# Kernel optimization log

Measured on AMD Instinct MI355X. Metric: run time of the kernel, lower is better.

The kernel has to match this reference:

```python
import jax, jax.numpy as jnp
import numpy as np

DIM = 1024
NUM_HEADS = 16
HEAD_DIM = DIM // NUM_HEADS
SCALE = HEAD_DIM ** -0.5


def setup_inputs() -> dict:
    key = jax.random.key(0)
    k1, k2, k3, k4 = jax.random.split(key, 4)
    x = jax.random.normal(k1, (4, 2048, DIM), dtype=jnp.float32)
    # torch nn.Linear(dim, 3*dim, bias=False): weight shape [3*dim, dim]
    w_qkv = jax.random.normal(k2, (3 * DIM, DIM), dtype=jnp.float32) * (DIM ** -0.5)
    # torch nn.Linear(dim, dim): weight [dim, dim], bias [dim]
    w_proj = jax.random.normal(k3, (DIM, DIM), dtype=jnp.float32) * (DIM ** -0.5)
    b_proj = jax.random.normal(k4, (DIM,), dtype=jnp.float32) * 0.01
    return {"x": x, "w_qkv": w_qkv, "w_proj": w_proj, "b_proj": b_proj}


def reference(x, w_qkv, w_proj, b_proj):
    B, N, C = x.shape
    # qkv: [B, N, 3*C] -> [3, B, H, N, Dh]
    qkv = (x @ w_qkv.T).reshape(B, N, 3, NUM_HEADS, HEAD_DIM)
    qkv = jnp.transpose(qkv, (2, 0, 3, 1, 4))
    q, k, v = qkv[0], qkv[1], qkv[2]
    # full score matrix, as in the original module
    attn = jnp.einsum("bhqd,bhkd->bhqk", q, k) * SCALE
    attn = jax.nn.softmax(attn, axis=-1)
    out = jnp.einsum("bhqk,bhkd->bhqd", attn, v)  # [B,H,N,Dh]
    out = jnp.transpose(out, (0, 2, 1, 3)).reshape(B, N, C)
    return out @ w_proj.T + b_proj
```

## Files before the change

kernel.cpp:

```cpp
#include <hip/hip_runtime.h>
#include <stdint.h>

#define DIM 1024
#define SEQ 2048
#define BATCH 4
#define ROWS (BATCH*SEQ)
#define QSCALE 0.1803368801111f

typedef __attribute__((ext_vector_type(8))) short bf16x8;
typedef __attribute__((ext_vector_type(4))) float f32x4;
typedef __attribute__((ext_vector_type(8))) _Float16 f16x8;
typedef __attribute__((ext_vector_type(2))) __fp16 fp16x2_raw;

#if __has_builtin(__builtin_amdgcn_exp2f)
#define EXP2F(x) __builtin_amdgcn_exp2f(x)
#else
#define EXP2F(x) __expf((x) * 0.69314718056f)
#endif

#define MFMA_BF16_K32(a,b,c) __builtin_amdgcn_mfma_f32_16x16x32_bf16(a,b,c,0,0,0)
#define MFMA_F16_K32(a,b,c)  __builtin_amdgcn_mfma_f32_16x16x32_f16(a,b,c,0,0,0)

__device__ __forceinline__ unsigned short f2bf(float f) {
  union { float f; unsigned int u; } v; v.f = f;
  unsigned int u = v.u;
  return (unsigned short)((u + 0x7FFFu + ((u >> 16) & 1u)) >> 16);
}

__device__ __forceinline__ unsigned short f2h(float f) {
  union { _Float16 h; unsigned short u; } v;
  v.h = (_Float16)f;
  return v.u;
}

__device__ __forceinline__ unsigned int pkrtz_bits(float lo, float hi) {
  union { fp16x2_raw h; unsigned int u; } v;
  v.h = __builtin_amdgcn_cvt_pkrtz(lo, hi);
  return v.u;
}

__device__ __forceinline__ void gload_lds16(const void* g, void* l) {
  __builtin_amdgcn_global_load_lds(
      (const __attribute__((address_space(1))) unsigned int*)g,
      (__attribute__((address_space(3))) unsigned int*)l,
      16, 0, 0);
}

__global__ void cast_all(const float* __restrict__ x,
                         const float* __restrict__ wq,
                         const float* __restrict__ wp,
                         unsigned short* __restrict__ xb,
                         unsigned short* __restrict__ wqb,
                         unsigned short* __restrict__ wpb) {
  const int i = (blockIdx.x * blockDim.x + threadIdx.x) * 4;
  const float* src;
  unsigned short* dst;
  int off;
  if (i < ROWS * DIM)                 { src = x;  dst = xb;  off = i; }
  else if (i < ROWS * DIM + 3 * DIM * DIM) { src = wq; dst = wqb; off = i - ROWS * DIM; }
  else                                { src = wp; dst = wpb; off = i - ROWS * DIM - 3 * DIM * DIM; }
  float4 f = *(const float4*)(src + off);
  ushort4 o;
  o.x = f2bf(f.x); o.y = f2bf(f.y); o.z = f2bf(f.z); o.w = f2bf(f.w);
  *(ushort4*)(dst + off) = o;
}

template<int SWAP>
__device__ __forceinline__ f32x4 mm(bf16x8 a, bf16x8 b, f32x4 c) {
  if constexpr (SWAP) return __builtin_amdgcn_mfma_f32_16x16x32_bf16(b, a, c, 0, 0, 0);
  else                return __builtin_amdgcn_mfma_f32_16x16x32_bf16(a, b, c, 0, 0, 0);
}

template<int SWAP, int NTX>
__global__ __launch_bounds__(512, 2) void gemm_qkv8(
    const unsigned short* __restrict__ A,
    const unsigned short* __restrict__ W,
    unsigned short* __restrict__ qb,
    unsigned short* __restrict__ kb,
    unsigned short* __restrict__ vtb) {
  constexpr int K = DIM;
  constexpr int NT = K / 64;
  constexpr int N0B = SWAP ? 0 : 2048;
  __shared__ unsigned short Al[2][256 * 64];
  __shared__ unsigned short Bl[2][256 * 64];

  const int tid  = threadIdx.x;
  const int wave = tid >> 6, lane = tid & 63;
  const int quad = lane >> 4, l16 = lane & 15;
  const int wm = wave >> 2, wn = wave & 3;

  constexpr int nwg = NTX * 32;
  int id = blockIdx.y * NTX + blockIdx.x;
  id = (id & 7) * (nwg >> 3) + (id >> 3);
  const int bx = id % NTX, by = id / NTX;
  const int m0 = by * 256, n0 = N0B + bx * 256;

  const int srow8 = lane >> 3;
  const int schk  = (lane & 7) ^ srow8;
  const unsigned short* Ast = A + (size_t)(m0 + wave * 8 + srow8) * K + (schk << 3);
  const unsigned short* Bst = W + (size_t)(n0 + wave * 8 + srow8) * K + (schk << 3);

  auto stg = [&](const unsigned short* g, int R0, int kt, unsigned short* l) {
    gload_lds16((const void*)(g + (size_t)R0 * K + kt),
                (void*)(l + (R0 + wave * 8) * 64));
  };
  auto ldf = [&](const unsigned short* base, int rb, int idx, int kk) -> bf16x8 {
    const int r = rb + idx * 16 + l16;
    return *(const bf16x8*)&base[r * 64 + (((kk * 4 + quad) ^ (l16 & 7)) << 3)];
  };

  f32x4 acc[8][4];
#pragma unroll
  for (int i = 0; i < 8; ++i)
#pragma unroll
    for (int j = 0; j < 4; ++j) acc[i][j] = (f32x4)0.f;

  stg(Ast, 0, 0, Al[0]);  stg(Ast, 128, 0, Al[0]);
  stg(Ast, 64, 0, Al[0]); stg(Ast, 192, 0, Al[0]);
  stg(Bst, 0, 0, Bl[0]);  stg(Bst, 64, 0, Bl[0]);
  stg(Bst, 128, 0, Bl[0]); stg(Bst, 192, 0, Bl[0]);
  stg(Ast, 0, 64, Al[1]);  stg(Ast, 128, 64, Al[1]);
  stg(Bst, 0, 64, Bl[1]);  stg(Bst, 64, 64, Bl[1]);
  stg(Ast, 64, 64, Al[1]); stg(Ast, 192, 64, Al[1]);
  asm volatile("s_waitcnt vmcnt(6)" ::: "memory");
  __builtin_amdgcn_s_barrier();

  bf16x8 af[4][2], bf[4][2];
  int buf = 0;
  for (int t = 0; t < NT; ++t, buf ^= 1) {
    const unsigned short* Ac = Al[buf];
    const unsigned short* Bc = Bl[buf];
    unsigned short* Asg = Al[buf];
    unsigned short* Bsg = Bl[buf];
    const int kt2 = (t + 2) * 64;

#pragma unroll
    for (int mi = 0; mi < 4; ++mi) {
      af[mi][0] = ldf(Ac, wm * 128, mi, 0);
      af[mi][1] = ldf(Ac, wm * 128, mi, 1);
    }
#pragma unroll
    for (int ni = 0; ni < 2; ++ni) {
      bf[ni][0] = ldf(Bc, wn * 64, ni, 0);
      bf[ni][1] = ldf(Bc, wn * 64, ni, 1);
    }
    if (t + 1 < NT) {
      stg(Bst, 128, (t + 1) * 64, Bl[buf ^ 1]);
      stg(Bst, 192, (t + 1) * 64, Bl[buf ^ 1]);
    }
    __builtin_amdgcn_s_barrier();
    asm volatile("s_waitcnt lgkmcnt(0)" ::: "memory");
    __builtin_amdgcn_s_setprio(1);
#pragma unroll
    for (int mi = 0; mi < 4; ++mi)
#pragma unroll
      for (int ni = 0; ni < 2; ++ni)
#pragma unroll
        for (int kk = 0; kk < 2; ++kk)
          acc[mi][ni] = mm<SWAP>(af[mi][kk], bf[ni][kk], acc[mi][ni]);
    __builtin_amdgcn_s_setprio(0);
    __builtin_amdgcn_s_barrier();

#pragma unroll
    for (int ni = 2; ni < 4; ++ni) {
      bf[ni][0] = ldf(Bc, wn * 64, ni, 0);
      bf[ni][1] = ldf(Bc, wn * 64, ni, 1);
    }
    if (t + 2 < NT) {
      stg(Ast, 0, kt2, Asg);
      stg(Ast, 128, kt2, Asg);
    }
    __builtin_amdgcn_s_barrier();
    asm volatile("s_waitcnt lgkmcnt(0)" ::: "memory");
    __builtin_amdgcn_s_setprio(1);
#pragma unroll
    for (int mi = 0; mi < 4; ++mi)
#pragma unroll
      for (int ni = 2; ni < 4; ++ni)
#pragma unroll
        for (int kk = 0; kk < 2; ++kk)
          acc[mi][ni] = mm<SWAP>(af[mi][kk], bf[ni][kk], acc[mi][ni]);
    __builtin_amdgcn_s_setprio(0);
    __builtin_amdgcn_s_barrier();

#pragma unroll
    for (int mi = 0; mi < 4; ++mi) {
      af[mi][0] = ldf(Ac, wm * 128, mi + 4, 0);
      af[mi][1] = ldf(Ac, wm * 128, mi + 4, 1);
    }
    if (t + 2 < NT) {
      stg(Bst, 0, kt2, Bsg);
      stg(Bst, 64, kt2, Bsg);
    }
    __builtin_amdgcn_s_barrier();
    asm volatile("s_waitcnt lgkmcnt(0)" ::: "memory");
    __builtin_amdgcn_s_setprio(1);
#pragma unroll
    for (int mi = 0; mi < 4; ++mi)
#pragma unroll
      for (int ni = 2; ni < 4; ++ni)
#pragma unroll
        for (int kk = 0; kk < 2; ++kk)
          acc[mi + 4][ni] = mm<SWAP>(af[mi][kk], bf[ni][kk], acc[mi + 4][ni]);
    __builtin_amdgcn_s_setprio(0);
    __builtin_amdgcn_s_barrier();

    if (t + 2 < NT) {
      stg(Ast, 64, kt2, Asg);
      stg(Ast, 192, kt2, Asg);
      asm volatile("s_waitcnt vmcnt(6)" ::: "memory");
    } else {
      asm volatile("s_waitcnt vmcnt(0)" ::: "memory");
    }
    __builtin_amdgcn_s_barrier();
    __builtin_amdgcn_s_setprio(1);
#pragma unroll
    for (int mi = 0; mi < 4; ++mi)
#pragma unroll
      for (int ni = 0; ni < 2; ++ni)
#pragma unroll
        for (int kk = 0; kk < 2; ++kk)
          acc[mi + 4][ni] = mm<SWAP>(af[mi][kk], bf[ni][kk], acc[mi + 4][ni]);
    __builtin_amdgcn_s_setprio(0);
    __builtin_amdgcn_s_barrier();
  }

  if constexpr (SWAP) {
    const float sc = (n0 < 1024) ? QSCALE : 1.f;
    unsigned short* base = (n0 < 1024) ? qb : kb;
#pragma unroll
    for (int mi = 0; mi < 8; ++mi) {
      const int tok = m0 + wm * 128 + mi * 16 + l16;
      const int b = tok >> 11, n = tok & 2047;
#pragma unroll
      for (int ni = 0; ni < 4; ++ni) {
        const int f0 = n0 + wn * 64 + ni * 16 + quad * 4;
        const int h = (f0 >> 6) & 15, d = f0 & 63;
        ushort4 o4;
        o4.x = f2bf(acc[mi][ni][0] * sc);
        o4.y = f2bf(acc[mi][ni][1] * sc);
        o4.z = f2bf(acc[mi][ni][2] * sc);
        o4.w = f2bf(acc[mi][ni][3] * sc);
        *(ushort4*)&base[((size_t)(b * 16 + h) * SEQ + n) * 64 + d] = o4;
      }
    }
  } else {
#pragma unroll
    for (int mi = 0; mi < 8; ++mi) {
      const int row = m0 + wm * 128 + mi * 16 + quad * 4;
      const int b = row >> 11, n = row & 2047;
#pragma unroll
      for (int ni = 0; ni < 4; ++ni) {
        const int col = n0 + wn * 64 + ni * 16 + l16;
        const int h = (col >> 6) & 15, d = col & 63;
        ushort4 o4;
        o4.x = f2h(acc[mi][ni][0]); o4.y = f2h(acc[mi][ni][1]);
        o4.z = f2h(acc[mi][ni][2]); o4.w = f2h(acc[mi][ni][3]);
        *(ushort4*)&vtb[((size_t)(b * 16 + h) * 64 + d) * SEQ + n] = o4;
      }
    }
  }
}

template<int EPI>
__global__ __launch_bounds__(512, 2) void gemm8_128x256(
    const unsigned short* __restrict__ A,
    const unsigned short* __restrict__ W,
    unsigned short* __restrict__ vtb,
    float* __restrict__ outp,
    const float* __restrict__ bias) {
  constexpr int K = DIM;
  constexpr int NT = K / 64;
  __shared__ unsigned short Al[2][128 * 64];
  __shared__ unsigned short Bl[2][256 * 64];

  const int tid  = threadIdx.x;
  const int wave = tid >> 6, lane = tid & 63;
  const int quad = lane >> 4, l16 = lane & 15;
  const int wm = wave >> 2, wn = wave & 3;

  int id = blockIdx.y * 4 + blockIdx.x;
  id = (id & 7) * 32 + (id >> 3);
  const int bx = id & 3, by = id >> 2;
  const int m0 = by * 128, n0 = bx * 256;

  const int srow8 = lane >> 3;
  const int schk  = (lane & 7) ^ srow8;
  const unsigned short* Ast = A + (size_t)(m0 + srow8) * K + (schk << 3);
  const unsigned short* Bst = W + (size_t)(n0 + srow8) * K + (schk << 3);

  auto stgA = [&](int kt, unsigned short* l, int R0, int R1) {
    const int rs = (wave < 4 ? R0 : R1) + (wave & 3) * 8;
    gload_lds16((const void*)(Ast + (size_t)rs * K + kt), (void*)(l + rs * 64));
  };
  auto stgB = [&](int kt, unsigned short* l, int R0, int R1) {
    const int rs = (wave < 4 ? R0 : R1) + (wave & 3) * 8;
    gload_lds16((const void*)(Bst + (size_t)rs * K + kt), (void*)(l + rs * 64));
  };
  auto ldf = [&](const unsigned short* base, int rb, int idx, int kk) -> bf16x8 {
    const int r = rb + idx * 16 + l16;
    return *(const bf16x8*)&base[r * 64 + (((kk * 4 + quad) ^ (l16 & 7)) << 3)];
  };

  f32x4 acc[4][4];
#pragma unroll
  for (int i = 0; i < 4; ++i)
#pragma unroll
    for (int j = 0; j < 4; ++j) acc[i][j] = (f32x4)0.f;

  stgA(0, Al[0], 0, 64);   stgA(0, Al[0], 32, 96);
  stgB(0, Bl[0], 0, 64);   stgB(0, Bl[0], 32, 96);
  stgB(0, Bl[0], 128, 192); stgB(0, Bl[0], 160, 224);
  stgA(64, Al[1], 0, 64);  stgA(64, Al[1], 32, 96);
  stgB(64, Bl[1], 0, 64);  stgB(64, Bl[1], 32, 96);
  asm volatile("s_waitcnt vmcnt(4)" ::: "memory");
  __builtin_amdgcn_s_barrier();

  bf16x8 af[2][2], bf[4][2];
  int buf = 0;
  for (int t = 0; t < NT; ++t, buf ^= 1) {
    const unsigned short* Ac = Al[buf];
    const unsigned short* Bc = Bl[buf];
    unsigned short* Asg = Al[buf];
    unsigned short* Bsg = Bl[buf];
    const int kt2 = (t + 2) * 64;

#pragma unroll
    for (int i = 0; i < 2; ++i) {
      af[i][0] = ldf(Ac, wm * 64, i, 0);
      af[i][1] = ldf(Ac, wm * 64, i, 1);
    }
#pragma unroll
    for (int ni = 0; ni < 2; ++ni) {
      bf[ni][0] = ldf(Bc, wn * 64, ni, 0);
      bf[ni][1] = ldf(Bc, wn * 64, ni, 1);
    }
    if (t + 1 < NT) {
      stgB((t + 1) * 64, Bl[buf ^ 1], 128, 192);
      stgB((t + 1) * 64, Bl[buf ^ 1], 160, 224);
    }
    __builtin_amdgcn_s_barrier();
    asm volatile("s_waitcnt lgkmcnt(0)" ::: "memory");
    __builtin_amdgcn_s_setprio(1);
#pragma unroll
    for (int mi = 0; mi < 2; ++mi)
#pragma unroll
      for (int ni = 0; ni < 2; ++ni)
#pragma unroll
        for (int kk = 0; kk < 2; ++kk)
          acc[mi][ni] = mm<0>(af[mi][kk], bf[ni][kk], acc[mi][ni]);
    __builtin_amdgcn_s_setprio(0);
    __builtin_amdgcn_s_barrier();

#pragma unroll
    for (int ni = 2; ni < 4; ++ni) {
      bf[ni][0] = ldf(Bc, wn * 64, ni, 0);
      bf[ni][1] = ldf(Bc, wn * 64, ni, 1);
    }
    if (t + 2 < NT) stgA(kt2, Asg, 0, 64);
    __builtin_amdgcn_s_barrier();
    asm volatile("s_waitcnt lgkmcnt(0)" ::: "memory");
    __builtin_amdgcn_s_setprio(1);
#pragma unroll
    for (int mi = 0; mi < 2; ++mi)
#pragma unroll
      for (int ni = 2; ni < 4; ++ni)
#pragma unroll
        for (int kk = 0; kk < 2; ++kk)
          acc[mi][ni] = mm<0>(af[mi][kk], bf[ni][kk], acc[mi][ni]);
    __builtin_amdgcn_s_setprio(0);
    __builtin_amdgcn_s_barrier();

#pragma unroll
    for (int i = 0; i < 2; ++i) {
      af[i][0] = ldf(Ac, wm * 64, i + 2, 0);
      af[i][1] = ldf(Ac, wm * 64, i + 2, 1);
    }
    if (t + 2 < NT) {
      stgB(kt2, Bsg, 0, 64);
      stgB(kt2, Bsg, 32, 96);
    }
    __builtin_amdgcn_s_barrier();
    asm volatile("s_waitcnt lgkmcnt(0)" ::: "memory");
    __builtin_amdgcn_s_setprio(1);
#pragma unroll
    for (int mi = 0; mi < 2; ++mi)
#pragma unroll
      for (int ni = 2; ni < 4; ++ni)
#pragma unroll
        for (int kk = 0; kk < 2; ++kk)
          acc[mi + 2][ni] = mm<0>(af[mi][kk], bf[ni][kk], acc[mi + 2][ni]);
    __builtin_amdgcn_s_setprio(0);
    __builtin_amdgcn_s_barrier();

    if (t + 2 < NT) {
      stgA(kt2, Asg, 32, 96);
      asm volatile("s_waitcnt vmcnt(4)" ::: "memory");
    } else {
      asm volatile("s_waitcnt vmcnt(0)" ::: "memory");
    }
    __builtin_amdgcn_s_barrier();
    __builtin_amdgcn_s_setprio(1);
#pragma unroll
    for (int mi = 0; mi < 2; ++mi)
#pragma unroll
      for (int ni = 0; ni < 2; ++ni)
#pragma unroll
        for (int kk = 0; kk < 2; ++kk)
          acc[mi + 2][ni] = mm<0>(af[mi][kk], bf[ni][kk], acc[mi + 2][ni]);
    __builtin_amdgcn_s_setprio(0);
    __builtin_amdgcn_s_barrier();
  }

  if constexpr (EPI == 0) {
#pragma unroll
    for (int mi = 0; mi < 4; ++mi) {
      const int row = m0 + wm * 64 + mi * 16 + quad * 4;
      const int b = row >> 11, n = row & 2047;
#pragma unroll
      for (int ni = 0; ni < 4; ++ni) {
        const int col = n0 + wn * 64 + ni * 16 + l16;
        const int h = (col >> 6) & 15, d = col & 63;
        ushort4 o4;
        o4.x = f2h(acc[mi][ni][0]); o4.y = f2h(acc[mi][ni][1]);
        o4.z = f2h(acc[mi][ni][2]); o4.w = f2h(acc[mi][ni][3]);
        *(ushort4*)&vtb[((size_t)(b * 16 + h) * 64 + d) * SEQ + n] = o4;
      }
    }
  } else {
#pragma unroll
    for (int mi = 0; mi < 4; ++mi) {
      const int row = m0 + wm * 64 + mi * 16 + quad * 4;
#pragma unroll
      for (int ni = 0; ni < 4; ++ni) {
        const int col = n0 + wn * 64 + ni * 16 + l16;
        const float bv = bias[col];
#pragma unroll
        for (int r = 0; r < 4; ++r)
          outp[(size_t)(row + r) * DIM + col] = acc[mi][ni][r] + bv;
      }
    }
  }
}

__global__ __launch_bounds__(512, 4) void attn_kernel(
    const unsigned short* __restrict__ qb,
    const unsigned short* __restrict__ kb,
    const unsigned short* __restrict__ vtb,
    unsigned short* __restrict__ out) {
  __shared__ unsigned short Kl[3][64 * 64];
  __shared__ unsigned short Vl[3][64 * 64];

  const int tid  = threadIdx.x;
  const int wave = tid >> 6, lane = tid & 63;
  const int quad = lane >> 4, l16 = lane & 15;
  const int bh    = blockIdx.x;
  const int qtile = blockIdx.y;
  const size_t qkbase = (size_t)bh * SEQ * 64;
  const int q0 = qtile * 256 + wave * 32;

  bf16x8 qf[2][2];
#pragma unroll
  for (int mi = 0; mi < 2; mi++)
#pragma unroll
    for (int kk = 0; kk < 2; kk++)
      qf[mi][kk] = *(const bf16x8*)&qb[qkbase + (size_t)(q0 + mi * 16 + l16) * 64 + kk * 32 + quad * 8];

  f32x4 o[2][4];
#pragma unroll
  for (int mi = 0; mi < 2; mi++)
#pragma unroll
    for (int nt = 0; nt < 4; nt++) o[mi][nt] = (f32x4)0.f;
  f32x4 lacc[2];
#pragma unroll
  for (int mi = 0; mi < 2; mi++) lacc[mi] = (f32x4)0.f;

  union { f16x8 v; unsigned int d[4]; } ones8;
#pragma unroll
  for (int j = 0; j < 4; j++) ones8.d[j] = 0x3C003C00u;

  const unsigned short* Kg = kb + qkbase;
  const unsigned short* Vg = vtb + (size_t)bh * 64 * SEQ;
  const int srow = tid >> 3;
  const int schk = tid & 7;
  const int swK = (srow & 3) | (((srow >> 3) & 1) << 2);
  const int swV = srow & 7;

  auto stage = [&](int kt, int b) {
    gload_lds16((const void*)(Kg + (size_t)(kt + srow) * 64 + (schk ^ swK) * 8),
                (void*)&Kl[b][wave * 512]);
    gload_lds16((const void*)(Vg + (size_t)srow * SEQ + kt + (schk ^ swV) * 8),
                (void*)&Vl[b][wave * 512]);
  };

  stage(0, 0);
  stage(64, 1);

  const int rbase = ((l16 >> 2) << 3) + (l16 & 3);
  const int sR = (l16 & 3) | (((l16 >> 2) & 1) << 2);

  int b0 = 0, b1 = 1, b2 = 2;
  for (int t = 0; t < 32; ++t) {
    if (t < 31) asm volatile("s_waitcnt vmcnt(2) lgkmcnt(0)" ::: "memory");
    else        asm volatile("s_waitcnt vmcnt(0) lgkmcnt(0)" ::: "memory");
    __builtin_amdgcn_s_barrier();
    if (t + 2 < 32) stage((t + 2) * 64, b2);

    const unsigned short* Kc = &Kl[b0][0];
    const unsigned short* Vc = &Vl[b0][0];

#pragma unroll
    for (int kk = 0; kk < 2; kk++) {
      bf16x8 kf[2][2];
#pragma unroll
      for (int T = 0; T < 2; T++) {
        const int R = kk * 32 + rbase + 4 * T;
        kf[T][0] = *(const bf16x8*)&Kc[R * 64 + ((quad ^ sR) << 3)];
        kf[T][1] = *(const bf16x8*)&Kc[R * 64 + (((4 + quad) ^ sR) << 3)];
      }
      f16x8 vf[4];
#pragma unroll
      for (int nt = 0; nt < 4; nt++) {
        const int vr = nt * 16 + l16;
        vf[nt] = *(const f16x8*)&Vc[vr * 64 + (((kk * 4 + quad) ^ (vr & 7)) << 3)];
      }
      __builtin_amdgcn_s_setprio(1);
#pragma unroll
      for (int mi = 0; mi < 2; mi++) {
        f32x4 s0 = (f32x4)0.f, s1 = (f32x4)0.f;
        s0 = MFMA_BF16_K32(kf[0][0], qf[mi][0], s0);
        s0 = MFMA_BF16_K32(kf[0][1], qf[mi][1], s0);
        s1 = MFMA_BF16_K32(kf[1][0], qf[mi][0], s1);
        s1 = MFMA_BF16_K32(kf[1][1], qf[mi][1], s1);
        union { f16x8 v; unsigned int d[4]; } pu;
        pu.d[0] = pkrtz_bits(EXP2F(s0[0]), EXP2F(s0[1]));
        pu.d[1] = pkrtz_bits(EXP2F(s0[2]), EXP2F(s0[3]));
        pu.d[2] = pkrtz_bits(EXP2F(s1[0]), EXP2F(s1[1]));
        pu.d[3] = pkrtz_bits(EXP2F(s1[2]), EXP2F(s1[3]));
        lacc[mi] = MFMA_F16_K32(pu.v, ones8.v, lacc[mi]);
#pragma unroll
        for (int nt = 0; nt < 4; nt++)
          o[mi][nt] = MFMA_F16_K32(pu.v, vf[nt], o[mi][nt]);
      }
      __builtin_amdgcn_s_setprio(0);
    }
    const int tmp = b0; b0 = b1; b1 = b2; b2 = tmp;
  }

  const int h = bh & 15, b = bh >> 4;
#pragma unroll
  for (int mi = 0; mi < 2; mi++) {
    float inv[4];
#pragma unroll
    for (int r = 0; r < 4; r++) inv[r] = 1.f / lacc[mi][r];
#pragma unroll
    for (int nt = 0; nt < 4; nt++)
#pragma unroll
      for (int r = 0; r < 4; r++)
        out[((size_t)(b * SEQ + q0 + mi * 16 + quad * 4 + r)) * DIM + h * 64 + nt * 16 + l16] =
            f2bf(o[mi][nt][r] * inv[r]);
  }
}

extern "C" void kernel_launch(void* const* d_in, const int* in_sizes, int n_in,
                              void* d_out, int out_size, void* d_ws, size_t ws_size,
                              hipStream_t stream) {
  const float* x      = (const float*)d_in[0];
  const float* w_qkv  = (const float*)d_in[1];
  const float* w_proj = (const float*)d_in[2];
  const float* b_proj = (const float*)d_in[3];
  float* outp = (float*)d_out;

  char* ws = (char*)d_ws;
  unsigned short* xb     = (unsigned short*)(ws);
  unsigned short* wqkvb  = (unsigned short*)(ws + (16u << 20));
  unsigned short* wprojb = (unsigned short*)(ws + (22u << 20));
  unsigned short* qb     = (unsigned short*)(ws + (24u << 20));
  unsigned short* kb     = (unsigned short*)(ws + (40u << 20));
  unsigned short* vtb    = (unsigned short*)(ws + (56u << 20));
  unsigned short* aout   = (unsigned short*)(ws + (72u << 20));

  const int total4 = (ROWS * DIM + 3 * DIM * DIM + DIM * DIM) / 4;
  cast_all<<<total4 / 256, 256, 0, stream>>>(x, w_qkv, w_proj, xb, wqkvb, wprojb);

  gemm_qkv8<1, 8><<<dim3(8, 32), 512, 0, stream>>>(xb, wqkvb, qb, kb, vtb);
  gemm8_128x256<0><<<dim3(4, 64), 512, 0, stream>>>(
      xb, wqkvb + (size_t)2048 * DIM, vtb, nullptr, nullptr);
  attn_kernel<<<dim3(64, 8), 512, 0, stream>>>(qb, kb, vtb, aout);
  gemm8_128x256<1><<<dim3(4, 64), 512, 0, stream>>>(
      aout, wprojb, nullptr, outp, b_proj);
}
```

Baseline: 258.2 us.

## Switch attention K/V staging to double-buffered 128-key tiles

The attention kernel now stages 128 keys per iteration into two LDS buffers instead of 64 keys into three. This halves the number of barriers and main-loop iterations, and each thread issues two async loads per operand. The prefetch depth drops from two tiles ahead to one, and the wait is now a full vmcnt(0) before every barrier. Launch bounds are lowered to 2 blocks per CU to match the larger LDS footprint, which reduces occupancy and latency hiding.

```diff
diff --git a/kernel.cpp b/kernel.cpp
--- a/kernel.cpp
+++ b/kernel.cpp
@@ -443,13 +443,13 @@
   }
 }
 
-__global__ __launch_bounds__(512, 4) void attn_kernel(
+__global__ __launch_bounds__(512, 2) void attn_kernel(
     const unsigned short* __restrict__ qb,
     const unsigned short* __restrict__ kb,
     const unsigned short* __restrict__ vtb,
     unsigned short* __restrict__ out) {
-  __shared__ unsigned short Kl[3][64 * 64];
-  __shared__ unsigned short Vl[3][64 * 64];
+  __shared__ unsigned short Kl[2][128 * 64];
+  __shared__ unsigned short Vl[2][64 * 128];
 
   const int tid  = threadIdx.x;
   const int wave = tid >> 6, lane = tid & 63;
@@ -463,8 +463,8 @@
 #pragma unroll
   for (int mi = 0; mi < 2; mi++)
 #pragma unroll
-    for (int kk = 0; kk < 2; kk++)
-      qf[mi][kk] = *(const bf16x8*)&qb[qkbase + (size_t)(q0 + mi * 16 + l16) * 64 + kk * 32 + quad * 8];
+    for (int dk = 0; dk < 2; dk++)
+      qf[mi][dk] = *(const bf16x8*)&qb[qkbase + (size_t)(q0 + mi * 16 + l16) * 64 + dk * 32 + quad * 8];
 
   f32x4 o[2][4];
 #pragma unroll
@@ -484,33 +484,35 @@
   const int srow = tid >> 3;
   const int schk = tid & 7;
   const int swK = (srow & 3) | (((srow >> 3) & 1) << 2);
-  const int swV = srow & 7;
+  const int vrow = tid >> 4;
+  const int vchk = tid & 15;
+  const int swV = vrow & 7;
 
   auto stage = [&](int kt, int b) {
-    gload_lds16((const void*)(Kg + (size_t)(kt + srow) * 64 + (schk ^ swK) * 8),
-                (void*)&Kl[b][wave * 512]);
-    gload_lds16((const void*)(Vg + (size_t)srow * SEQ + kt + (schk ^ swV) * 8),
-                (void*)&Vl[b][wave * 512]);
+#pragma unroll
+    for (int p = 0; p < 2; p++) {
+      gload_lds16((const void*)(Kg + (size_t)(kt + p * 64 + srow) * 64 + (schk ^ swK) * 8),
+                  (void*)&Kl[b][(p * 64 + wave * 8) * 64]);
+      gload_lds16((const void*)(Vg + (size_t)(p * 32 + vrow) * SEQ + kt + ((vchk ^ swV) << 3)),
+                  (void*)&Vl[b][(p * 32 + wave * 4) * 128]);
+    }
   };
 
   stage(0, 0);
-  stage(64, 1);
 
   const int rbase = ((l16 >> 2) << 3) + (l16 & 3);
   const int sR = (l16 & 3) | (((l16 >> 2) & 1) << 2);
 
-  int b0 = 0, b1 = 1, b2 = 2;
-  for (int t = 0; t < 32; ++t) {
-    if (t < 31) asm volatile("s_waitcnt vmcnt(2) lgkmcnt(0)" ::: "memory");
-    else        asm volatile("s_waitcnt vmcnt(0) lgkmcnt(0)" ::: "memory");
-    __builtin_amdgcn_s_barrier();
-    if (t + 2 < 32) stage((t + 2) * 64, b2);
-
-    const unsigned short* Kc = &Kl[b0][0];
-    const unsigned short* Vc = &Vl[b0][0];
-
-#pragma unroll
-    for (int kk = 0; kk < 2; kk++) {
+  for (int t = 0; t < 16; ++t) {
+    asm volatile("s_waitcnt vmcnt(0) lgkmcnt(0)" ::: "memory");
+    __builtin_amdgcn_s_barrier();
+    if (t + 1 < 16) stage((t + 1) * 128, (t + 1) & 1);
+
+    const unsigned short* Kc = &Kl[t & 1][0];
+    const unsigned short* Vc = &Vl[t & 1][0];
+
+#pragma unroll
+    for (int kk = 0; kk < 4; kk++) {
       bf16x8 kf[2][2];
 #pragma unroll
       for (int T = 0; T < 2; T++) {
@@ -522,7 +524,7 @@
 #pragma unroll
       for (int nt = 0; nt < 4; nt++) {
         const int vr = nt * 16 + l16;
-        vf[nt] = *(const f16x8*)&Vc[vr * 64 + (((kk * 4 + quad) ^ (vr & 7)) << 3)];
+        vf[nt] = *(const f16x8*)&Vc[vr * 128 + (((kk * 4 + quad) ^ (vr & 7)) << 3)];
       }
       __builtin_amdgcn_s_setprio(1);
 #pragma unroll
@@ -544,7 +546,6 @@
       }
       __builtin_amdgcn_s_setprio(0);
     }
-    const int tmp = b0; b0 = b1; b1 = b2; b2 = tmp;
   }
 
   const int h = bh & 15, b = bh >> 4;
```

Result: no change. 258.4 us (+0.1%).
